# Kernel optimization log

Hardware: AMD Instinct MI355X
Metric: run time of the kernel (lower is better)

The kernel has to match this reference:

```python
import jax, jax.numpy as jnp
import numpy as np

N_NODES = 100000
N_EDGES = 1600000
D_IN = 256
D_OUT = 128


def _gcn_norm(edge_index, num_nodes):
    # Add self-loops and compute symmetric normalization D^-1/2 A D^-1/2 (PyG GCNConv default).
    src, dst = edge_index[0], edge_index[1]
    loop = jnp.arange(num_nodes, dtype=edge_index.dtype)
    src = jnp.concatenate([src, loop])
    dst = jnp.concatenate([dst, loop])
    deg = jax.ops.segment_sum(jnp.ones_like(dst, dtype=jnp.float32), dst, num_segments=num_nodes)
    dinv = jnp.where(deg > 0, jax.lax.rsqrt(jnp.maximum(deg, 1.0)), 0.0)
    norm = dinv[src] * dinv[dst]  # [E + N]
    return src, dst, norm


def _gcn_conv(x, W, b, src, dst, norm, num_nodes):
    h = x @ W  # [N, d_out] transform first (d_out <= d_in keeps message traffic low)
    msg = h[src] * norm[:, None]  # [E+N, d_out] gather + scale
    out = jax.ops.segment_sum(msg, dst, num_segments=num_nodes)  # scatter-add
    return out + b


def setup_inputs() -> dict:
    key = jax.random.key(0)
    ks = jax.random.split(key, 8)
    x = jax.random.normal(ks[0], (N_NODES, D_IN), dtype=jnp.float32)
    edge_index = jax.random.randint(ks[1], (2, N_EDGES), 0, N_NODES, dtype=jnp.int64)
    s = 0.05
    return {
        "x": x,
        "edge_index": edge_index,
        "W1": jax.random.normal(ks[2], (D_IN, D_OUT), dtype=jnp.float32) * s,
        "b1": jnp.zeros((D_OUT,), dtype=jnp.float32),
        "W_mu": jax.random.normal(ks[3], (D_OUT, D_OUT), dtype=jnp.float32) * s,
        "b_mu": jnp.zeros((D_OUT,), dtype=jnp.float32),
        "W_ls": jax.random.normal(ks[4], (D_OUT, D_OUT), dtype=jnp.float32) * s,
        "b_ls": jnp.zeros((D_OUT,), dtype=jnp.float32),
    }


def reference(x, edge_index, W1, b1, W_mu, b_mu, W_ls, b_ls):
    num_nodes = x.shape[0]
    src, dst, norm = _gcn_norm(edge_index, num_nodes)
    h = jax.nn.relu(_gcn_conv(x, W1, b1, src, dst, norm, num_nodes))
    mu = _gcn_conv(h, W_mu, b_mu, src, dst, norm, num_nodes)
    logstd = _gcn_conv(h, W_ls, b_ls, src, dst, norm, num_nodes)
    return (mu, logstd)
```

## Files before the change

kernel.cpp:

```cpp
#include <hip/hip_runtime.h>
#include <hip/hip_bf16.h>
#include <hip/hip_fp16.h>

typedef __attribute__((ext_vector_type(8))) short short8;
typedef __attribute__((ext_vector_type(8))) _Float16 f16x8;
typedef __attribute__((ext_vector_type(4))) float f32x4;

#define EPB 16384

__global__ __launch_bounds__(256) void k_lhist(const int* __restrict__ dst, int* __restrict__ histT,
                                               int nE, int nblk, int nbins) {
  __shared__ int c[1024];
  int tid = threadIdx.x;
  for (int i = tid; i < nbins; i += 256) c[i] = 0;
  __syncthreads();
  int blk = blockIdx.x;
  int e0 = blk * EPB;
  int e1 = min(nE, e0 + EPB);
  if (e1 - e0 == EPB) {
#pragma unroll
    for (int it = 0; it < EPB / 1024; ++it) {
      int4 d = *(const int4*)(dst + e0 + it * 1024 + tid * 4);
      atomicAdd(&c[d.x >> 7], 1);
      atomicAdd(&c[d.y >> 7], 1);
      atomicAdd(&c[d.z >> 7], 1);
      atomicAdd(&c[d.w >> 7], 1);
    }
  } else {
    for (int i = e0 + tid; i < e1; i += 256) atomicAdd(&c[dst[i] >> 7], 1);
  }
  __syncthreads();
  for (int i = tid; i < nbins; i += 256) histT[i * nblk + blk] = c[i];
}

__global__ __launch_bounds__(256) void k_lscatter(
    const int* __restrict__ src, const int* __restrict__ dst, const int* __restrict__ subPtr,
    int* __restrict__ binned, int nE, int nblk, int nbins) {
  __shared__ int cur[1024];
  int tid = threadIdx.x;
  int blk = blockIdx.x;
  for (int i = tid; i < nbins; i += 256) cur[i] = subPtr[i * nblk + blk];
  __syncthreads();
  int e0 = blk * EPB;
  int e1 = min(nE, e0 + EPB);
  if (e1 - e0 == EPB) {
#pragma unroll
    for (int it = 0; it < EPB / 1024; ++it) {
      int base = e0 + it * 1024 + tid * 4;
      int4 s = *(const int4*)(src + base);
      int4 d = *(const int4*)(dst + base);
      int p0 = atomicAdd(&cur[d.x >> 7], 1);
      int p1 = atomicAdd(&cur[d.y >> 7], 1);
      int p2 = atomicAdd(&cur[d.z >> 7], 1);
      int p3 = atomicAdd(&cur[d.w >> 7], 1);
      binned[p0] = s.x | ((d.x & 127) << 20);
      binned[p1] = s.y | ((d.y & 127) << 20);
      binned[p2] = s.z | ((d.z & 127) << 20);
      binned[p3] = s.w | ((d.w & 127) << 20);
    }
  } else {
    for (int i = e0 + tid; i < e1; i += 256) {
      int d = dst[i];
      int pos = atomicAdd(&cur[d >> 7], 1);
      binned[pos] = src[i] | ((d & 127) << 20);
    }
  }
}


__global__ __launch_bounds__(256) void k_bin_finish(
    const int* __restrict__ binned, const int* __restrict__ subPtr,
    int* __restrict__ cnt, int* __restrict__ rowptr, float* __restrict__ dinv,
    int* __restrict__ col, int nE, int nblk, int nbins, int n) {
  __shared__ int c128[128];
  __shared__ int scan128[128];
  __shared__ int cur128[128];
  int b = blockIdx.x;
  int tid = threadIdx.x;
  if (tid < 128) c128[tid] = 0;
  __syncthreads();
  int s0 = subPtr[b * nblk];
  int s1 = (b + 1 < nbins) ? subPtr[(b + 1) * nblk] : nE;
  for (int i = s0 + tid; i < s1; i += 256)
    atomicAdd(&c128[(binned[i] >> 20) & 127], 1);
  __syncthreads();
  if (tid < 128) scan128[tid] = c128[tid];
  __syncthreads();
  for (int off = 1; off < 128; off <<= 1) {
    int t = 0;
    if (tid < 128 && tid >= off) t = scan128[tid - off];
    __syncthreads();
    if (tid < 128) scan128[tid] += t;
    __syncthreads();
  }
  if (tid < 128) {
    int v = c128[tid];
    int excl = scan128[tid] - v;
    int rp = s0 + excl;
    int idx = (b << 7) + tid;
    if (idx < n) {
      cnt[idx] = v;
      rowptr[idx] = rp;
      dinv[idx] = rsqrtf((float)(v + 1));
    }
    cur128[tid] = rp;
  }
  __syncthreads();
  for (int i = s0 + tid; i < s1; i += 256) {
    int e = binned[i];
    int pos = atomicAdd(&cur128[(e >> 20) & 127], 1);
    col[pos] = e & 0xFFFFF;
  }
}


__global__ void k_blocksum(const int* __restrict__ cnt, int* __restrict__ bsum, int n) {
  __shared__ int red[256];
  int tid = threadIdx.x;
  int base = blockIdx.x * 1024 + tid * 4;
  int s = 0;
#pragma unroll
  for (int i = 0; i < 4; i++) { int idx = base + i; if (idx < n) s += cnt[idx]; }
  red[tid] = s;
  __syncthreads();
  for (int off = 128; off > 0; off >>= 1) {
    if (tid < off) red[tid] += red[tid + off];
    __syncthreads();
  }
  if (tid == 0) bsum[blockIdx.x] = red[0];
}

__global__ void k_scan_bsum(int* __restrict__ bsum, int nb) {
  __shared__ int s[128];
  int tid = threadIdx.x;
  int v = (tid < nb) ? bsum[tid] : 0;
  s[tid] = v;
  __syncthreads();
  for (int off = 1; off < 128; off <<= 1) {
    int t = (tid >= off) ? s[tid - off] : 0;
    __syncthreads();
    s[tid] += t;
    __syncthreads();
  }
  if (tid < nb) bsum[tid] = s[tid] - v;
}

__global__ void k_scan_final(const int* __restrict__ cnt, const int* __restrict__ bsum,
                             int* __restrict__ rowptr, int n) {
  __shared__ int tsum[256];
  int tid = threadIdx.x;
  int base = blockIdx.x * 1024 + tid * 4;
  int v[4]; int s = 0;
#pragma unroll
  for (int i = 0; i < 4; i++) { v[i] = (base + i < n) ? cnt[base + i] : 0; s += v[i]; }
  tsum[tid] = s;
  __syncthreads();
  for (int off = 1; off < 256; off <<= 1) {
    int t = (tid >= off) ? tsum[tid - off] : 0;
    __syncthreads();
    tsum[tid] += t;
    __syncthreads();
  }
  int run = bsum[blockIdx.x] + tsum[tid] - s;
#pragma unroll
  for (int i = 0; i < 4; i++) {
    int idx = base + i;
    if (idx < n) { rowptr[idx] = run; run += v[i]; }
  }
}


__global__ void k_prep_w(const float* __restrict__ W1,
                         const float* __restrict__ Wmu, const float* __restrict__ Wls,
                         const float* __restrict__ bmu, const float* __restrict__ bls,
                         __half* __restrict__ W1T, __half* __restrict__ WcT,
                         float* __restrict__ bcat) {
  int i = blockIdx.x * blockDim.x + threadIdx.x;
  if (i < 128 * 256) {
    int n = i >> 8, k = i & 255;
    W1T[i] = __float2half(W1[k * 128 + n]);
  } else if (i < 2 * 128 * 256) {
    int j = i - 128 * 256;
    int n = j >> 7, k = j & 127;
    float f = (n < 128) ? Wmu[k * 128 + n] : Wls[k * 128 + (n - 128)];
    WcT[j] = __float2half(f);
  } else if (i < 2 * 128 * 256 + 256) {
    int n = i - 2 * 128 * 256;
    bcat[n] = (n < 128) ? bmu[n] : bls[n - 128];
  }
}


#define LP 40

__global__ __launch_bounds__(256) void k_gemm_mfma(
    const float* __restrict__ Av, const __half* __restrict__ WT,
    __half* __restrict__ out0, int M, int K) {
  __shared__ _Float16 As[128 * LP];
  __shared__ _Float16 Bs[128 * LP];

  const int tid = threadIdx.x;
  const int lane = tid & 63;
  const int wv = tid >> 6;
  const int wr = wv >> 1, wc = wv & 1;
  const int rsel = lane >> 4;
  const int rrow = lane & 15;
  const int row0 = blockIdx.x * 128;

  f32x4 acc[4][4];
#pragma unroll
  for (int m = 0; m < 4; m++)
#pragma unroll
    for (int n = 0; n < 4; n++) acc[m][n] = (f32x4){0.f, 0.f, 0.f, 0.f};

  const int srow = tid >> 1;
  const int skh = (tid & 1) * 16;

  for (int k0 = 0; k0 < K; k0 += 32) {
    if (row0 + srow < M) {
      const float* src = Av + (size_t)(row0 + srow) * K + k0 + skh;
      float4 f0 = *(const float4*)(src);
      float4 f1 = *(const float4*)(src + 4);
      float4 f2 = *(const float4*)(src + 8);
      float4 f3 = *(const float4*)(src + 12);
      f16x8 v0, v1;
      v0[0]=(_Float16)f0.x; v0[1]=(_Float16)f0.y; v0[2]=(_Float16)f0.z; v0[3]=(_Float16)f0.w;
      v0[4]=(_Float16)f1.x; v0[5]=(_Float16)f1.y; v0[6]=(_Float16)f1.z; v0[7]=(_Float16)f1.w;
      v1[0]=(_Float16)f2.x; v1[1]=(_Float16)f2.y; v1[2]=(_Float16)f2.z; v1[3]=(_Float16)f2.w;
      v1[4]=(_Float16)f3.x; v1[5]=(_Float16)f3.y; v1[6]=(_Float16)f3.z; v1[7]=(_Float16)f3.w;
      *(f16x8*)&As[srow * LP + skh]     = v0;
      *(f16x8*)&As[srow * LP + skh + 8] = v1;
    } else {
      f16x8 z = (f16x8){0,0,0,0,0,0,0,0};
      *(f16x8*)&As[srow * LP + skh] = z; *(f16x8*)&As[srow * LP + skh + 8] = z;
    }
    {
      const _Float16* s = (const _Float16*)WT + (size_t)srow * K + k0 + skh;
      *(f16x8*)&Bs[srow * LP + skh]     = *(const f16x8*)s;
      *(f16x8*)&Bs[srow * LP + skh + 8] = *(const f16x8*)(s + 8);
    }
    __syncthreads();

    f16x8 fa[4], fb[4];
#pragma unroll
    for (int m = 0; m < 4; m++)
      fa[m] = *(f16x8*)&As[(wr * 64 + m * 16 + rrow) * LP + rsel * 8];
#pragma unroll
    for (int n = 0; n < 4; n++)
      fb[n] = *(f16x8*)&Bs[(wc * 64 + n * 16 + rrow) * LP + rsel * 8];
#pragma unroll
    for (int m = 0; m < 4; m++)
#pragma unroll
      for (int n = 0; n < 4; n++)
        acc[m][n] = __builtin_amdgcn_mfma_f32_16x16x32_f16(fa[m], fb[n], acc[m][n], 0, 0, 0);
    __syncthreads();
  }

#pragma unroll
  for (int n = 0; n < 4; n++) {
    int c = wc * 64 + n * 16 + rrow;
#pragma unroll
    for (int m = 0; m < 4; m++) {
      f32x4 v = acc[m][n];
#pragma unroll
      for (int r = 0; r < 4; r++) {
        int row = row0 + wr * 64 + m * 16 + rsel * 4 + r;
        if (row < M) out0[(size_t)row * 128 + c] = __float2half(v[r]);
      }
    }
  }
}


__global__ __launch_bounds__(256) void k_spmm_h(
    const __half* __restrict__ in, const int* __restrict__ rowptr,
    const int* __restrict__ cnt, const int* __restrict__ col,
    const float* __restrict__ dinv,
    const float* __restrict__ bias, __half* __restrict__ out,
    int n, int use_bias, int relu_out) {
  int node = blockIdx.x * 4 + (threadIdx.x >> 6);
  if (node >= n) return;
  int lane = threadIdx.x & 63;

  const __half2* inp = (const __half2*)in;
  float di = dinv[node];
  float2 v = __half22float2(inp[(size_t)node * 64 + lane]);
  float accx = di * v.x;
  float accy = di * v.y;

  int beg = rowptr[node];
  int m = cnt[node];
  int i = 0;
  for (; i + 8 <= m; i += 8) {
    int c[8];
#pragma unroll
    for (int j = 0; j < 8; j++) c[j] = col[beg + i + j];
    float e[8];
#pragma unroll
    for (int j = 0; j < 8; j++) e[j] = dinv[c[j]];
    float2 u[8];
#pragma unroll
    for (int j = 0; j < 8; j++) u[j] = __half22float2(inp[(size_t)c[j] * 64 + lane]);
#pragma unroll
    for (int j = 0; j < 8; j++) { accx += e[j] * u[j].x; accy += e[j] * u[j].y; }
  }
  if (i < m) {
    int c[8];
#pragma unroll
    for (int j = 0; j < 8; j++) c[j] = col[(i + j < m) ? (beg + i + j) : beg];
    float e[8];
#pragma unroll
    for (int j = 0; j < 8; j++) e[j] = (i + j < m) ? dinv[c[j]] : 0.f;
    float2 u[8];
#pragma unroll
    for (int j = 0; j < 8; j++) u[j] = __half22float2(inp[(size_t)c[j] * 64 + lane]);
#pragma unroll
    for (int j = 0; j < 8; j++) { accx += e[j] * u[j].x; accy += e[j] * u[j].y; }
  }
  accx *= di;
  accy *= di;
  if (use_bias) {
    accx += bias[2 * lane];
    accy += bias[2 * lane + 1];
  }
  if (relu_out) {
    accx = fmaxf(accx, 0.f);
    accy = fmaxf(accy, 0.f);
  }
  ((__half2*)(out + (size_t)node * 128))[lane] = __floats2half2_rn(accx, accy);
}


__global__ __launch_bounds__(256) void k_spmm_gemm(
    const __half* __restrict__ in, const int* __restrict__ rowptr,
    const int* __restrict__ cnt, const int* __restrict__ col,
    const float* __restrict__ dinv,
    const __half* __restrict__ WcT, const float* __restrict__ bcat,
    float* __restrict__ out0, float* __restrict__ out1, int n) {
  __shared__ _Float16 gt[16 * 128];
  const int tid = threadIdx.x;
  const int lane = tid & 63;
  const int w = tid >> 6;
  const __half2* inp = (const __half2*)in;

  for (int q = 0; q < 4; q++) {
    int li = w * 4 + q;
    int node = blockIdx.x * 16 + li;
    float accx = 0.f, accy = 0.f;
    if (node < n) {
      float di = dinv[node];
      float2 v = __half22float2(inp[(size_t)node * 64 + lane]);
      accx = di * v.x;
      accy = di * v.y;
      int beg = rowptr[node];
      int m = cnt[node];
      int i = 0;
      for (; i + 8 <= m; i += 8) {
        int c[8];
#pragma unroll
        for (int j = 0; j < 8; j++) c[j] = col[beg + i + j];
        float e[8];
#pragma unroll
        for (int j = 0; j < 8; j++) e[j] = dinv[c[j]];
        float2 u[8];
#pragma unroll
        for (int j = 0; j < 8; j++) u[j] = __half22float2(inp[(size_t)c[j] * 64 + lane]);
#pragma unroll
        for (int j = 0; j < 8; j++) { accx += e[j] * u[j].x; accy += e[j] * u[j].y; }
      }
      if (i < m) {
        int c[8];
#pragma unroll
        for (int j = 0; j < 8; j++) c[j] = col[(i + j < m) ? (beg + i + j) : beg];
        float e[8];
#pragma unroll
        for (int j = 0; j < 8; j++) e[j] = (i + j < m) ? dinv[c[j]] : 0.f;
        float2 u[8];
#pragma unroll
        for (int j = 0; j < 8; j++) u[j] = __half22float2(inp[(size_t)c[j] * 64 + lane]);
#pragma unroll
        for (int j = 0; j < 8; j++) { accx += e[j] * u[j].x; accy += e[j] * u[j].y; }
      }
      accx *= di;
      accy *= di;
    }
    int slot = (lane >> 2) ^ (li & 7);
    *(__half2*)((char*)gt + li * 256 + slot * 16 + (lane & 3) * 4) =
        __floats2half2_rn(accx, accy);
  }
  __syncthreads();

  const int lr = lane & 15;
  const int lk = lane >> 4;
  f16x8 a[4];
#pragma unroll
  for (int ks = 0; ks < 4; ks++) {
    int slot = (ks * 4 + lk) ^ (lr & 7);
    a[ks] = *(const f16x8*)((const char*)gt + lr * 256 + slot * 16);
  }
#pragma unroll
  for (int ct = 0; ct < 4; ct++) {
    int colg = (w * 4 + ct) * 16 + lr;
    f32x4 acc = (f32x4){0.f, 0.f, 0.f, 0.f};
#pragma unroll
    for (int ks = 0; ks < 4; ks++) {
      f16x8 b = *(const f16x8*)((const _Float16*)WcT + (size_t)colg * 128 + ks * 32 + lk * 8);
      acc = __builtin_amdgcn_mfma_f32_16x16x32_f16(a[ks], b, acc, 0, 0, 0);
    }
    float badd = bcat[colg];
    float* dst = out0;
    int c = colg;
    if (c >= 128) { dst = out1; c -= 128; }
#pragma unroll
    for (int r = 0; r < 4; r++) {
      int node = blockIdx.x * 16 + lk * 4 + r;
      if (node < n) dst[(size_t)node * 128 + c] = acc[r] + badd;
    }
  }
}


extern "C" void kernel_launch(void* const* d_in, const int* in_sizes, int n_in,
                              void* d_out, int out_size, void* d_ws, size_t ws_size,
                              hipStream_t stream) {
  const float* x   = (const float*)d_in[0];
  const int*   ei  = (const int*)d_in[1];
  const float* W1  = (const float*)d_in[2];
  const float* b1  = (const float*)d_in[3];
  const float* Wmu = (const float*)d_in[4];
  const float* bmu = (const float*)d_in[5];
  const float* Wls = (const float*)d_in[6];
  const float* bls = (const float*)d_in[7];

  int N = in_sizes[0] / 256;
  int E = in_sizes[1] / 2;
  const int* src = ei;
  const int* dst = ei + E;

  int NBINS = (N + 127) >> 7;
  int NBLK  = (E + EPB - 1) / EPB;
  int NS    = NBINS * NBLK;

  char* ws = (char*)d_ws;
  size_t o = 0;
  auto alloc = [&](size_t b) { size_t c = o; o = (o + b + 511) & ~(size_t)511; return c; };
  int*   cnt     = (int*)(ws + alloc((size_t)N * 4));
  int*   rowptr  = (int*)(ws + alloc((size_t)N * 4));
  float* dinv    = (float*)(ws + alloc((size_t)N * 4));
  int*   bsum    = (int*)(ws + alloc(512));
  int*   histT   = (int*)(ws + alloc((size_t)NS * 4));
  int*   subPtr  = (int*)(ws + alloc((size_t)NS * 4));
  int*   col     = (int*)(ws + alloc((size_t)E * 4));
  int*   binned  = (int*)(ws + alloc((size_t)E * 4));
  __half* W1T  = (__half*)(ws + alloc(128 * 256 * 2));
  __half* WcT  = (__half*)(ws + alloc(256 * 128 * 2));
  float*  bcat = (float*)(ws + alloc(256 * 4));
  __half* h0   = (__half*)(ws + alloc((size_t)N * 128 * 2));
  __half* hBuf = (__half*)(ws + alloc((size_t)N * 128 * 2));

  float* outMu = (float*)d_out;
  float* outLs = outMu + (size_t)N * 128;

  int nbScanS = (NS + 1023) / 1024;

  k_lhist<<<NBLK, 256, 0, stream>>>(dst, histT, E, NBLK, NBINS);
  k_blocksum<<<nbScanS, 256, 0, stream>>>(histT, bsum, NS);
  k_scan_bsum<<<1, 128, 0, stream>>>(bsum, nbScanS);
  k_scan_final<<<nbScanS, 256, 0, stream>>>(histT, bsum, subPtr, NS);
  k_lscatter<<<NBLK, 256, 0, stream>>>(src, dst, subPtr, binned, E, NBLK, NBINS);
  k_bin_finish<<<NBINS, 256, 0, stream>>>(binned, subPtr, cnt, rowptr, dinv, col,
                                          E, NBLK, NBINS, N);

  k_prep_w<<<(2 * 128 * 256 + 256 + 255) / 256, 256, 0, stream>>>(
      W1, Wmu, Wls, bmu, bls, W1T, WcT, bcat);

  k_gemm_mfma<<<(N + 127) / 128, 256, 0, stream>>>(x, W1T, h0, N, 256);
  k_spmm_h<<<(N + 3) / 4, 256, 0, stream>>>(h0, rowptr, cnt, col, dinv, b1, hBuf, N, 1, 1);
  k_spmm_gemm<<<(N + 15) / 16, 256, 0, stream>>>(
      hBuf, rowptr, cnt, col, dinv, WcT, bcat, outMu, outLs, N);
}
```

Baseline: 289.9 us.

## Fuse edge binning into one pass with fixed-capacity bins; widen GEMM blocks

Histogram and scatter now run in one kernel. Each block reserves space in a per-bin region of fixed capacity by doing a global atomicAdd on a bin cursor, so the three prefix-scan kernels and the separate scatter pass go away. The CSR arrays become padded: each bin owns CAP slots, and rowptr points into that layout. The intent is fewer launches and fewer passes over the edge list. The catch is that any bin holding more than CAP edges would overflow silently, and edge order within a bin is no longer deterministic. Separately, the feature GEMM now uses 512-thread blocks with 8 waves, each computing a 64x32 tile, to raise the number of waves per block.

```diff
diff --git a/kernel.cpp b/kernel.cpp
--- a/kernel.cpp
+++ b/kernel.cpp
@@ -7,15 +7,17 @@
 typedef __attribute__((ext_vector_type(4))) float f32x4;
 
 #define EPB 16384
-
-__global__ __launch_bounds__(256) void k_lhist(const int* __restrict__ dst, int* __restrict__ histT,
-                                               int nE, int nblk, int nbins) {
+#define CAP_SHIFT 13
+#define CAP (1 << CAP_SHIFT)
+
+__global__ __launch_bounds__(256) void k_fused_scatter(
+    const int* __restrict__ src, const int* __restrict__ dst,
+    int* __restrict__ binCursor, int* __restrict__ binned, int nE, int nbins) {
   __shared__ int c[1024];
   int tid = threadIdx.x;
   for (int i = tid; i < nbins; i += 256) c[i] = 0;
   __syncthreads();
-  int blk = blockIdx.x;
-  int e0 = blk * EPB;
+  int e0 = blockIdx.x * EPB;
   int e1 = min(nE, e0 + EPB);
   if (e1 - e0 == EPB) {
 #pragma unroll
@@ -30,29 +32,22 @@
     for (int i = e0 + tid; i < e1; i += 256) atomicAdd(&c[dst[i] >> 7], 1);
   }
   __syncthreads();
-  for (int i = tid; i < nbins; i += 256) histT[i * nblk + blk] = c[i];
-}
-
-__global__ __launch_bounds__(256) void k_lscatter(
-    const int* __restrict__ src, const int* __restrict__ dst, const int* __restrict__ subPtr,
-    int* __restrict__ binned, int nE, int nblk, int nbins) {
-  __shared__ int cur[1024];
-  int tid = threadIdx.x;
-  int blk = blockIdx.x;
-  for (int i = tid; i < nbins; i += 256) cur[i] = subPtr[i * nblk + blk];
-  __syncthreads();
-  int e0 = blk * EPB;
-  int e1 = min(nE, e0 + EPB);
+  for (int i = tid; i < nbins; i += 256) {
+    int v = c[i];
+    int base = v ? atomicAdd(&binCursor[i], v) : 0;
+    c[i] = (i << CAP_SHIFT) + base;
+  }
+  __syncthreads();
   if (e1 - e0 == EPB) {
 #pragma unroll
     for (int it = 0; it < EPB / 1024; ++it) {
       int base = e0 + it * 1024 + tid * 4;
       int4 s = *(const int4*)(src + base);
       int4 d = *(const int4*)(dst + base);
-      int p0 = atomicAdd(&cur[d.x >> 7], 1);
-      int p1 = atomicAdd(&cur[d.y >> 7], 1);
-      int p2 = atomicAdd(&cur[d.z >> 7], 1);
-      int p3 = atomicAdd(&cur[d.w >> 7], 1);
+      int p0 = atomicAdd(&c[d.x >> 7], 1);
+      int p1 = atomicAdd(&c[d.y >> 7], 1);
+      int p2 = atomicAdd(&c[d.z >> 7], 1);
+      int p3 = atomicAdd(&c[d.w >> 7], 1);
       binned[p0] = s.x | ((d.x & 127) << 20);
       binned[p1] = s.y | ((d.y & 127) << 20);
       binned[p2] = s.z | ((d.z & 127) << 20);
@@ -61,7 +56,7 @@
   } else {
     for (int i = e0 + tid; i < e1; i += 256) {
       int d = dst[i];
-      int pos = atomicAdd(&cur[d >> 7], 1);
+      int pos = atomicAdd(&c[d >> 7], 1);
       binned[pos] = src[i] | ((d & 127) << 20);
     }
   }
@@ -69,9 +64,9 @@
 
 
 __global__ __launch_bounds__(256) void k_bin_finish(
-    const int* __restrict__ binned, const int* __restrict__ subPtr,
+    const int* __restrict__ binned, const int* __restrict__ binCnt,
     int* __restrict__ cnt, int* __restrict__ rowptr, float* __restrict__ dinv,
-    int* __restrict__ col, int nE, int nblk, int nbins, int n) {
+    int* __restrict__ col, int nbins, int n) {
   __shared__ int c128[128];
   __shared__ int scan128[128];
   __shared__ int cur128[128];
@@ -79,8 +74,8 @@
   int tid = threadIdx.x;
   if (tid < 128) c128[tid] = 0;
   __syncthreads();
-  int s0 = subPtr[b * nblk];
-  int s1 = (b + 1 < nbins) ? subPtr[(b + 1) * nblk] : nE;
+  int s0 = b << CAP_SHIFT;
+  int s1 = s0 + binCnt[b];
   for (int i = s0 + tid; i < s1; i += 256)
     atomicAdd(&c128[(binned[i] >> 20) & 127], 1);
   __syncthreads();
@@ -95,8 +90,7 @@
   }
   if (tid < 128) {
     int v = c128[tid];
-    int excl = scan128[tid] - v;
-    int rp = s0 + excl;
+    int rp = s0 + scan128[tid] - v;
     int idx = (b << 7) + tid;
     if (idx < n) {
       cnt[idx] = v;
@@ -110,62 +104,6 @@
     int e = binned[i];
     int pos = atomicAdd(&cur128[(e >> 20) & 127], 1);
     col[pos] = e & 0xFFFFF;
-  }
-}
-
-
-__global__ void k_blocksum(const int* __restrict__ cnt, int* __restrict__ bsum, int n) {
-  __shared__ int red[256];
-  int tid = threadIdx.x;
-  int base = blockIdx.x * 1024 + tid * 4;
-  int s = 0;
-#pragma unroll
-  for (int i = 0; i < 4; i++) { int idx = base + i; if (idx < n) s += cnt[idx]; }
-  red[tid] = s;
-  __syncthreads();
-  for (int off = 128; off > 0; off >>= 1) {
-    if (tid < off) red[tid] += red[tid + off];
-    __syncthreads();
-  }
-  if (tid == 0) bsum[blockIdx.x] = red[0];
-}
-
-__global__ void k_scan_bsum(int* __restrict__ bsum, int nb) {
-  __shared__ int s[128];
-  int tid = threadIdx.x;
-  int v = (tid < nb) ? bsum[tid] : 0;
-  s[tid] = v;
-  __syncthreads();
-  for (int off = 1; off < 128; off <<= 1) {
-    int t = (tid >= off) ? s[tid - off] : 0;
-    __syncthreads();
-    s[tid] += t;
-    __syncthreads();
-  }
-  if (tid < nb) bsum[tid] = s[tid] - v;
-}
-
-__global__ void k_scan_final(const int* __restrict__ cnt, const int* __restrict__ bsum,
-                             int* __restrict__ rowptr, int n) {
-  __shared__ int tsum[256];
-  int tid = threadIdx.x;
-  int base = blockIdx.x * 1024 + tid * 4;
-  int v[4]; int s = 0;
-#pragma unroll
-  for (int i = 0; i < 4; i++) { v[i] = (base + i < n) ? cnt[base + i] : 0; s += v[i]; }
-  tsum[tid] = s;
-  __syncthreads();
-  for (int off = 1; off < 256; off <<= 1) {
-    int t = (tid >= off) ? tsum[tid - off] : 0;
-    __syncthreads();
-    tsum[tid] += t;
-    __syncthreads();
-  }
-  int run = bsum[blockIdx.x] + tsum[tid] - s;
-#pragma unroll
-  for (int i = 0; i < 4; i++) {
-    int idx = base + i;
-    if (idx < n) { rowptr[idx] = run; run += v[i]; }
   }
 }
 
@@ -193,7 +131,7 @@
 
 #define LP 40
 
-__global__ __launch_bounds__(256) void k_gemm_mfma(
+__global__ __launch_bounds__(512) void k_gemm_mfma(
     const float* __restrict__ Av, const __half* __restrict__ WT,
     __half* __restrict__ out0, int M, int K) {
   __shared__ _Float16 As[128 * LP];
@@ -202,63 +140,54 @@
   const int tid = threadIdx.x;
   const int lane = tid & 63;
   const int wv = tid >> 6;
-  const int wr = wv >> 1, wc = wv & 1;
+  const int wr = wv >> 2, wc = wv & 3;
   const int rsel = lane >> 4;
   const int rrow = lane & 15;
   const int row0 = blockIdx.x * 128;
 
-  f32x4 acc[4][4];
+  f32x4 acc[4][2];
 #pragma unroll
   for (int m = 0; m < 4; m++)
 #pragma unroll
-    for (int n = 0; n < 4; n++) acc[m][n] = (f32x4){0.f, 0.f, 0.f, 0.f};
-
-  const int srow = tid >> 1;
-  const int skh = (tid & 1) * 16;
+    for (int n = 0; n < 2; n++) acc[m][n] = (f32x4){0.f, 0.f, 0.f, 0.f};
+
+  const int srow = tid >> 2;
+  const int skh = (tid & 3) * 8;
 
   for (int k0 = 0; k0 < K; k0 += 32) {
     if (row0 + srow < M) {
       const float* src = Av + (size_t)(row0 + srow) * K + k0 + skh;
       float4 f0 = *(const float4*)(src);
       float4 f1 = *(const float4*)(src + 4);
-      float4 f2 = *(const float4*)(src + 8);
-      float4 f3 = *(const float4*)(src + 12);
-      f16x8 v0, v1;
+      f16x8 v0;
       v0[0]=(_Float16)f0.x; v0[1]=(_Float16)f0.y; v0[2]=(_Float16)f0.z; v0[3]=(_Float16)f0.w;
       v0[4]=(_Float16)f1.x; v0[5]=(_Float16)f1.y; v0[6]=(_Float16)f1.z; v0[7]=(_Float16)f1.w;
-      v1[0]=(_Float16)f2.x; v1[1]=(_Float16)f2.y; v1[2]=(_Float16)f2.z; v1[3]=(_Float16)f2.w;
-      v1[4]=(_Float16)f3.x; v1[5]=(_Float16)f3.y; v1[6]=(_Float16)f3.z; v1[7]=(_Float16)f3.w;
-      *(f16x8*)&As[srow * LP + skh]     = v0;
-      *(f16x8*)&As[srow * LP + skh + 8] = v1;
+      *(f16x8*)&As[srow * LP + skh] = v0;
     } else {
-      f16x8 z = (f16x8){0,0,0,0,0,0,0,0};
-      *(f16x8*)&As[srow * LP + skh] = z; *(f16x8*)&As[srow * LP + skh + 8] = z;
-    }
-    {
-      const _Float16* s = (const _Float16*)WT + (size_t)srow * K + k0 + skh;
-      *(f16x8*)&Bs[srow * LP + skh]     = *(const f16x8*)s;
-      *(f16x8*)&Bs[srow * LP + skh + 8] = *(const f16x8*)(s + 8);
-    }
+      *(f16x8*)&As[srow * LP + skh] = (f16x8){0,0,0,0,0,0,0,0};
+    }
+    *(f16x8*)&Bs[srow * LP + skh] =
+        *(const f16x8*)((const _Float16*)WT + (size_t)srow * K + k0 + skh);
     __syncthreads();
 
-    f16x8 fa[4], fb[4];
+    f16x8 fa[4], fb[2];
 #pragma unroll
     for (int m = 0; m < 4; m++)
       fa[m] = *(f16x8*)&As[(wr * 64 + m * 16 + rrow) * LP + rsel * 8];
 #pragma unroll
-    for (int n = 0; n < 4; n++)
-      fb[n] = *(f16x8*)&Bs[(wc * 64 + n * 16 + rrow) * LP + rsel * 8];
+    for (int n = 0; n < 2; n++)
+      fb[n] = *(f16x8*)&Bs[(wc * 32 + n * 16 + rrow) * LP + rsel * 8];
 #pragma unroll
     for (int m = 0; m < 4; m++)
 #pragma unroll
-      for (int n = 0; n < 4; n++)
+      for (int n = 0; n < 2; n++)
         acc[m][n] = __builtin_amdgcn_mfma_f32_16x16x32_f16(fa[m], fb[n], acc[m][n], 0, 0, 0);
     __syncthreads();
   }
 
 #pragma unroll
-  for (int n = 0; n < 4; n++) {
-    int c = wc * 64 + n * 16 + rrow;
+  for (int n = 0; n < 2; n++) {
+    int c = wc * 32 + n * 16 + rrow;
 #pragma unroll
     for (int m = 0; m < 4; m++) {
       f32x4 v = acc[m][n];
@@ -439,19 +368,16 @@
 
   int NBINS = (N + 127) >> 7;
   int NBLK  = (E + EPB - 1) / EPB;
-  int NS    = NBINS * NBLK;
 
   char* ws = (char*)d_ws;
   size_t o = 0;
   auto alloc = [&](size_t b) { size_t c = o; o = (o + b + 511) & ~(size_t)511; return c; };
-  int*   cnt     = (int*)(ws + alloc((size_t)N * 4));
-  int*   rowptr  = (int*)(ws + alloc((size_t)N * 4));
-  float* dinv    = (float*)(ws + alloc((size_t)N * 4));
-  int*   bsum    = (int*)(ws + alloc(512));
-  int*   histT   = (int*)(ws + alloc((size_t)NS * 4));
-  int*   subPtr  = (int*)(ws + alloc((size_t)NS * 4));
-  int*   col     = (int*)(ws + alloc((size_t)E * 4));
-  int*   binned  = (int*)(ws + alloc((size_t)E * 4));
+  int*   cnt       = (int*)(ws + alloc((size_t)N * 4));
+  int*   rowptr    = (int*)(ws + alloc((size_t)N * 4));
+  float* dinv      = (float*)(ws + alloc((size_t)N * 4));
+  int*   binCursor = (int*)(ws + alloc((size_t)NBINS * 4));
+  int*   col       = (int*)(ws + alloc((size_t)NBINS * CAP * 4));
+  int*   binned    = (int*)(ws + alloc((size_t)NBINS * CAP * 4));
   __half* W1T  = (__half*)(ws + alloc(128 * 256 * 2));
   __half* WcT  = (__half*)(ws + alloc(256 * 128 * 2));
   float*  bcat = (float*)(ws + alloc(256 * 4));
@@ -461,20 +387,15 @@
   float* outMu = (float*)d_out;
   float* outLs = outMu + (size_t)N * 128;
 
-  int nbScanS = (NS + 1023) / 1024;
-
-  k_lhist<<<NBLK, 256, 0, stream>>>(dst, histT, E, NBLK, NBINS);
-  k_blocksum<<<nbScanS, 256, 0, stream>>>(histT, bsum, NS);
-  k_scan_bsum<<<1, 128, 0, stream>>>(bsum, nbScanS);
-  k_scan_final<<<nbScanS, 256, 0, stream>>>(histT, bsum, subPtr, NS);
-  k_lscatter<<<NBLK, 256, 0, stream>>>(src, dst, subPtr, binned, E, NBLK, NBINS);
-  k_bin_finish<<<NBINS, 256, 0, stream>>>(binned, subPtr, cnt, rowptr, dinv, col,
-                                          E, NBLK, NBINS, N);
+  hipMemsetAsync(binCursor, 0, (size_t)NBINS * 4, stream);
+  k_fused_scatter<<<NBLK, 256, 0, stream>>>(src, dst, binCursor, binned, E, NBINS);
+  k_bin_finish<<<NBINS, 256, 0, stream>>>(binned, binCursor, cnt, rowptr, dinv, col,
+                                          NBINS, N);
 
   k_prep_w<<<(2 * 128 * 256 + 256 + 255) / 256, 256, 0, stream>>>(
       W1, Wmu, Wls, bmu, bls, W1T, WcT, bcat);
 
-  k_gemm_mfma<<<(N + 127) / 128, 256, 0, stream>>>(x, W1T, h0, N, 256);
+  k_gemm_mfma<<<(N + 127) / 128, 512, 0, stream>>>(x, W1T, h0, N, 256);
   k_spmm_h<<<(N + 3) / 4, 256, 0, stream>>>(h0, rowptr, cnt, col, dinv, b1, hBuf, N, 1, 1);
   k_spmm_gemm<<<(N + 15) / 16, 256, 0, stream>>>(
       hBuf, rowptr, cnt, col, dinv, WcT, bcat, outMu, outLs, N);
```

New measurement: 277.4 us, median of 2. 1.04x faster.
